# Kernel optimization log

Hardware: AMD Instinct MI355X
Metric: run time of the kernel (lower is better)

Reference implementation:

```python
import jax, jax.numpy as jnp
import numpy as np

WS = 7   # w_size
K = 9    # k_neighbors


def setup_inputs() -> dict:
    key = jax.random.key(0)
    ks = jax.random.split(key, 6)
    B, C, H, W = 16, 64, 112, 112
    Cf = C // 4
    return {
        'x_in': jax.random.normal(ks[0], (B, C, H, W), jnp.float32),
        'Wf': jax.random.normal(ks[1], (Cf, C), jnp.float32) / np.sqrt(C).astype(np.float32),
        'bf': jnp.zeros((Cf,), jnp.float32),
        'Wp': jax.random.normal(ks[2], (C, Cf), jnp.float32) / np.sqrt(Cf).astype(np.float32),
        'bp': jnp.zeros((C,), jnp.float32),
        'W1': jax.random.normal(ks[3], (4, 2), jnp.float32) / np.sqrt(2.0).astype(np.float32),
        'b1': jnp.zeros((4,), jnp.float32),
        'W2': jax.random.normal(ks[4], (1, 4), jnp.float32) / 2.0,
        'b2': jnp.zeros((1,), jnp.float32),
        'sigma': jnp.asarray(4.0, jnp.float32),
        'alpha': jnp.asarray(0.5, jnp.float32),
    }


def reference(x_in, Wf, bf, Wp, bp, W1, b1, W2, b2, sigma, alpha):
    B, C, H, W = x_in.shape
    w, h = H // WS, W // WS                      # per-window spatial dims
    Bp, N = B * WS * WS, w * h                   # num windows, nodes per window
    # window partition: b c (Wg w) (Hg h) -> (b Wg Hg) c w h
    x = x_in.reshape(B, C, WS, w, WS, h).transpose(0, 2, 4, 1, 3, 5).reshape(Bp, C, w, h)
    # 1x1 conv f: dim -> dim//4
    f = jnp.einsum('bchw,oc->bohw', x, Wf) + bf[None, :, None, None]
    Cf = f.shape[1]
    xf = f.reshape(Bp, Cf, N).transpose(0, 2, 1)          # [Bp, N, Cf] node features
    # all-pairs cosine similarity (torch eps=1e-8)
    xn = xf / jnp.maximum(jnp.linalg.norm(xf, axis=-1, keepdims=True), 1e-8)
    sim_feat = jnp.einsum('bnc,bmc->bnm', xn, xn)         # [Bp, N, N]
    # spatial gaussian similarity
    ii, jj = jnp.meshgrid(jnp.arange(w), jnp.arange(h), indexing='ij')
    coords = jnp.stack([ii, jj], -1).reshape(N, 2).astype(jnp.float32)
    dist = jnp.sqrt(jnp.sum((coords[:, None] - coords[None]) ** 2, -1))
    sim_dist = jnp.exp(-dist ** 2 / (2.0 * sigma ** 2))   # [N, N]
    combined = alpha * sim_feat + (1.0 - alpha) * sim_dist[None]
    _, idx = jax.lax.top_k(combined, K)                   # [Bp, N, K] neighbor ids
    # gather neighbor messages; edges of node n are exactly its K top-k columns
    msg = xf[jnp.arange(Bp)[:, None, None], idx]          # [Bp, N, K, Cf]
    sf = jnp.take_along_axis(sim_feat, idx, axis=-1)      # edge cosine sim
    sd = sim_dist[jnp.arange(N)[:, None], idx]            # edge spatial sim
    pair = jnp.stack([sf, sd], -1)                        # [Bp, N, K, 2]
    hdn = jax.nn.silu(pair @ W1.T + b1)
    wgt = jax.nn.sigmoid(hdn @ W2.T + b2)[..., 0]         # [Bp, N, K]
    # scatter_add over edge_index[0] == per-source sum over its K edges
    wn = wgt / (jnp.sum(wgt, -1, keepdims=True) + 1e-12)
    out = jnp.einsum('bnk,bnkc->bnc', wn, msg)            # [Bp, N, Cf]
    out = out.reshape(Bp, w, h, Cf).transpose(0, 3, 1, 2)
    # window un-partition: (b Wg Hg) c w h -> b c (Wg w) (Hg h)
    out = out.reshape(B, WS, WS, Cf, w, h).transpose(0, 3, 1, 4, 2, 5).reshape(B, Cf, H, W)
    # 1x1 conv p: dim//4 -> dim, then flatten(2)
    y = jnp.einsum('bchw,oc->bohw', out, Wp) + bp[None, :, None, None]
    return y.reshape(B, C, H * W)
```

## Files before the change

kernel.cpp:

```cpp
#include <hip/hip_runtime.h>
#include <math.h>

#define CC    64
#define CF    16
#define NPIX  256
#define KK    9
#define HWQ   12544
#define WWQ   112

__global__ __launch_bounds__(256) void gnn_fused(
    const float* __restrict__ x_in, const float* __restrict__ Wf,
    const float* __restrict__ bf,   const float* __restrict__ Wp,
    const float* __restrict__ bp,   const float* __restrict__ W1,
    const float* __restrict__ b1,   const float* __restrict__ W2,
    const float* __restrict__ b2,   const float* __restrict__ sigma_p,
    const float* __restrict__ alpha_p, float* __restrict__ y)
{
    __shared__ float s_xf[NPIX][CF];
    __shared__ float s_xn[NPIX][CF];
    __shared__ float s_W[CC * CF];
    __shared__ float s_table[451];
    __shared__ float s_bias[CC];

    const int bpi = blockIdx.x;
    const int bb  = bpi / 49;
    const int ssb = bpi % 49;
    const int s1  = ssb / 7, s2 = ssb % 7;
    const int tid = threadIdx.x;
    const int pi  = tid >> 4, pj = tid & 15;
    const int gy  = s1 * 16 + pi, gx = s2 * 16 + pj;

    const float alpha = alpha_p[0];
    const float oma   = 1.0f - alpha;
    const float sig   = sigma_p[0];
    const float denom = 2.0f * sig * sig;

    for (int t = tid; t < CF * CC; t += NPIX) s_W[t] = Wf[t];
    if (tid < CF) s_bias[tid] = bf[tid];
    for (int t = tid; t < 451; t += NPIX) {
        float dd = sqrtf((float)t);
        s_table[t] = expf((-(dd * dd)) / denom);
    }
    float W1r[8], b1r[4], W2r[4];
    #pragma unroll
    for (int h = 0; h < 8; ++h) W1r[h] = W1[h];
    #pragma unroll
    for (int h = 0; h < 4; ++h) { b1r[h] = b1[h]; W2r[h] = W2[h]; }
    const float b2r = b2[0];
    __syncthreads();

    const float* xb = x_in + (size_t)bb * CC * HWQ + (size_t)gy * WWQ + gx;
    float fv[CF];
    #pragma unroll
    for (int o = 0; o < CF; ++o) fv[o] = 0.0f;
    for (int c = 0; c < CC; ++c) {
        float xv = xb[(size_t)c * HWQ];
        #pragma unroll
        for (int o = 0; o < CF; ++o)
            fv[o] = fmaf(xv, s_W[o * CC + c], fv[o]);
    }
    #pragma unroll
    for (int o = 0; o < CF; ++o) fv[o] += s_bias[o];

    float ss2 = 0.0f;
    #pragma unroll
    for (int o = 0; o < CF; ++o) ss2 = fmaf(fv[o], fv[o], ss2);
    float nrm = fmaxf(sqrtf(ss2), 1e-8f);

    float xnr[CF];
    #pragma unroll
    for (int o = 0; o < CF; ++o) {
        xnr[o] = fv[o] / nrm;
        s_xf[tid][o] = fv[o];
        s_xn[tid][o] = xnr[o];
    }
    __syncthreads();

    float tv[KK]; int ti[KK];
    #pragma unroll
    for (int k = 0; k < KK; ++k) { tv[k] = -INFINITY; ti[k] = 0; }

    for (int m = 0; m < NPIX; ++m) {
        const float4* xm4 = reinterpret_cast<const float4*>(&s_xn[m][0]);
        float4 a0 = xm4[0], a1 = xm4[1], a2 = xm4[2], a3 = xm4[3];
        float dot = 0.0f;
        dot = fmaf(xnr[0],  a0.x, dot); dot = fmaf(xnr[1],  a0.y, dot);
        dot = fmaf(xnr[2],  a0.z, dot); dot = fmaf(xnr[3],  a0.w, dot);
        dot = fmaf(xnr[4],  a1.x, dot); dot = fmaf(xnr[5],  a1.y, dot);
        dot = fmaf(xnr[6],  a1.z, dot); dot = fmaf(xnr[7],  a1.w, dot);
        dot = fmaf(xnr[8],  a2.x, dot); dot = fmaf(xnr[9],  a2.y, dot);
        dot = fmaf(xnr[10], a2.z, dot); dot = fmaf(xnr[11], a2.w, dot);
        dot = fmaf(xnr[12], a3.x, dot); dot = fmaf(xnr[13], a3.y, dot);
        dot = fmaf(xnr[14], a3.z, dot); dot = fmaf(xnr[15], a3.w, dot);

        int di = pi - (m >> 4);
        int dj = pj - (m & 15);
        float sd = s_table[di * di + dj * dj];
        float comb = __fadd_rn(__fmul_rn(alpha, dot), __fmul_rn(oma, sd));

        if (comb > tv[KK - 1]) {
            float cv = comb; int ci = m;
            #pragma unroll
            for (int t = KK - 1; t >= 0; --t) {
                bool g = (cv > tv[t]);
                float ov = tv[t]; int oi = ti[t];
                if (g) {
                    if (t + 1 < KK) { tv[t + 1] = ov; ti[t + 1] = oi; }
                    tv[t] = cv; ti[t] = ci;
                }
            }
        }
    }

    float wk[KK];
    float wsum = 0.0f;
    #pragma unroll
    for (int k = 0; k < KK; ++k) {
        int m = ti[k];
        int di = pi - (m >> 4);
        int dj = pj - (m & 15);
        float sd = s_table[di * di + dj * dj];
        float sf = (tv[k] - __fmul_rn(oma, sd)) / alpha;
        float hsum = b2r;
        #pragma unroll
        for (int h = 0; h < 4; ++h) {
            float z  = fmaf(sf, W1r[2 * h], fmaf(sd, W1r[2 * h + 1], b1r[h]));
            float sg = 1.0f / (1.0f + expf(-z));
            hsum = fmaf(z * sg, W2r[h], hsum);
        }
        float wg = 1.0f / (1.0f + expf(-hsum));
        wk[k] = wg;
        wsum += wg;
    }
    wsum += 1e-12f;

    float outv[CF];
    #pragma unroll
    for (int o = 0; o < CF; ++o) outv[o] = 0.0f;
    #pragma unroll
    for (int k = 0; k < KK; ++k) {
        float wn = wk[k] / wsum;
        int m = ti[k];
        const float4* xf4 = reinterpret_cast<const float4*>(&s_xf[m][0]);
        float4 m0 = xf4[0], m1 = xf4[1], m2 = xf4[2], m3 = xf4[3];
        outv[0]  = fmaf(wn, m0.x, outv[0]);  outv[1]  = fmaf(wn, m0.y, outv[1]);
        outv[2]  = fmaf(wn, m0.z, outv[2]);  outv[3]  = fmaf(wn, m0.w, outv[3]);
        outv[4]  = fmaf(wn, m1.x, outv[4]);  outv[5]  = fmaf(wn, m1.y, outv[5]);
        outv[6]  = fmaf(wn, m1.z, outv[6]);  outv[7]  = fmaf(wn, m1.w, outv[7]);
        outv[8]  = fmaf(wn, m2.x, outv[8]);  outv[9]  = fmaf(wn, m2.y, outv[9]);
        outv[10] = fmaf(wn, m2.z, outv[10]); outv[11] = fmaf(wn, m2.w, outv[11]);
        outv[12] = fmaf(wn, m3.x, outv[12]); outv[13] = fmaf(wn, m3.y, outv[13]);
        outv[14] = fmaf(wn, m3.z, outv[14]); outv[15] = fmaf(wn, m3.w, outv[15]);
    }

    __syncthreads();
    for (int t = tid; t < CC * CF; t += NPIX) s_W[t] = Wp[t];
    if (tid < CC) s_bias[tid] = bp[tid];
    __syncthreads();

    float* yb = y + (size_t)bb * CC * HWQ + (size_t)gy * WWQ + gx;
    for (int o = 0; o < CC; ++o) {
        float acc = 0.0f;
        #pragma unroll
        for (int c = 0; c < CF; ++c)
            acc = fmaf(outv[c], s_W[o * CF + c], acc);
        yb[(size_t)o * HWQ] = acc + s_bias[o];
    }
}

extern "C" void kernel_launch(void* const* d_in, const int* in_sizes, int n_in,
                              void* d_out, int out_size, void* d_ws, size_t ws_size,
                              hipStream_t stream) {
    const float* x_in  = (const float*)d_in[0];
    const float* Wf    = (const float*)d_in[1];
    const float* bf    = (const float*)d_in[2];
    const float* Wp    = (const float*)d_in[3];
    const float* bp    = (const float*)d_in[4];
    const float* W1    = (const float*)d_in[5];
    const float* b1    = (const float*)d_in[6];
    const float* W2    = (const float*)d_in[7];
    const float* b2    = (const float*)d_in[8];
    const float* sigma = (const float*)d_in[9];
    const float* alpha = (const float*)d_in[10];
    float* y = (float*)d_out;

    gnn_fused<<<784, 256, 0, stream>>>(x_in, Wf, bf, Wp, bp, W1, b1, W2, b2,
                                       sigma, alpha, y);
}
```

Baseline: 147.8 us.

## Split each window across two blocks and use branchless med3 top-k insertion

Each 256-node window now runs on two 128-thread blocks. Both blocks recompute the full window's 1x1 projection, and each block handles top-k and output for half the nodes. The raw-feature shared array is dropped: normalized features are stored with per-node norms and the norm is multiplied back during aggregation. The top-k insertion becomes a branchless fmed3/select network, the spatial loop is split into row and column parts, and the Wp reads are vectorized. This trades doubled projection work and doubled x_in reads for twice as many blocks, less shared memory and shorter insertion chains.

```diff
diff --git a/kernel.cpp b/kernel.cpp
--- a/kernel.cpp
+++ b/kernel.cpp
@@ -7,8 +7,9 @@
 #define KK    9
 #define HWQ   12544
 #define WWQ   112
-
-__global__ __launch_bounds__(256) void gnn_fused(
+#define BLK   128
+
+__global__ __launch_bounds__(BLK) void gnn_fused(
     const float* __restrict__ x_in, const float* __restrict__ Wf,
     const float* __restrict__ bf,   const float* __restrict__ Wp,
     const float* __restrict__ bp,   const float* __restrict__ W1,
@@ -16,28 +17,28 @@
     const float* __restrict__ b2,   const float* __restrict__ sigma_p,
     const float* __restrict__ alpha_p, float* __restrict__ y)
 {
-    __shared__ float s_xf[NPIX][CF];
     __shared__ float s_xn[NPIX][CF];
+    __shared__ float s_nrm[NPIX];
     __shared__ float s_W[CC * CF];
     __shared__ float s_table[451];
     __shared__ float s_bias[CC];
 
-    const int bpi = blockIdx.x;
-    const int bb  = bpi / 49;
-    const int ssb = bpi % 49;
-    const int s1  = ssb / 7, s2 = ssb % 7;
-    const int tid = threadIdx.x;
-    const int pi  = tid >> 4, pj = tid & 15;
-    const int gy  = s1 * 16 + pi, gx = s2 * 16 + pj;
+    const int bid  = blockIdx.x;
+    const int tile = bid >> 1;
+    const int hlf  = bid & 1;
+    const int bb   = tile / 49;
+    const int ssb  = tile % 49;
+    const int s1   = ssb / 7, s2 = ssb % 7;
+    const int tid  = threadIdx.x;
 
     const float alpha = alpha_p[0];
     const float oma   = 1.0f - alpha;
     const float sig   = sigma_p[0];
     const float denom = 2.0f * sig * sig;
 
-    for (int t = tid; t < CF * CC; t += NPIX) s_W[t] = Wf[t];
+    for (int t = tid; t < CF * CC; t += BLK) s_W[t] = Wf[t];
     if (tid < CF) s_bias[tid] = bf[tid];
-    for (int t = tid; t < 451; t += NPIX) {
+    for (int t = tid; t < 451; t += BLK) {
         float dd = sqrtf((float)t);
         s_table[t] = expf((-(dd * dd)) / denom);
     }
@@ -49,65 +50,106 @@
     const float b2r = b2[0];
     __syncthreads();
 
-    const float* xb = x_in + (size_t)bb * CC * HWQ + (size_t)gy * WWQ + gx;
-    float fv[CF];
-    #pragma unroll
-    for (int o = 0; o < CF; ++o) fv[o] = 0.0f;
-    for (int c = 0; c < CC; ++c) {
-        float xv = xb[(size_t)c * HWQ];
-        #pragma unroll
-        for (int o = 0; o < CF; ++o)
-            fv[o] = fmaf(xv, s_W[o * CC + c], fv[o]);
-    }
-    #pragma unroll
-    for (int o = 0; o < CF; ++o) fv[o] += s_bias[o];
-
-    float ss2 = 0.0f;
-    #pragma unroll
-    for (int o = 0; o < CF; ++o) ss2 = fmaf(fv[o], fv[o], ss2);
-    float nrm = fmaxf(sqrtf(ss2), 1e-8f);
+    #pragma unroll
+    for (int half = 0; half < 2; ++half) {
+        const int p   = tid + half * BLK;
+        const int ppi = p >> 4, ppj = p & 15;
+        const int pgy = s1 * 16 + ppi, pgx = s2 * 16 + ppj;
+        const float* xb = x_in + (size_t)bb * CC * HWQ + (size_t)pgy * WWQ + pgx;
+        float fv[CF];
+        #pragma unroll
+        for (int o = 0; o < CF; ++o) fv[o] = 0.0f;
+        for (int c = 0; c < CC; ++c) {
+            float xv = xb[(size_t)c * HWQ];
+            #pragma unroll
+            for (int o = 0; o < CF; ++o)
+                fv[o] = fmaf(xv, s_W[o * CC + c], fv[o]);
+        }
+        #pragma unroll
+        for (int o = 0; o < CF; ++o) fv[o] += s_bias[o];
+
+        float ss2 = 0.0f;
+        #pragma unroll
+        for (int o = 0; o < CF; ++o) ss2 = fmaf(fv[o], fv[o], ss2);
+        float nrm = fmaxf(sqrtf(ss2), 1e-8f);
+        #pragma unroll
+        for (int o = 0; o < CF; ++o) s_xn[p][o] = fv[o] / nrm;
+        s_nrm[p] = nrm;
+    }
+    __syncthreads();
+
+    const int r  = hlf * BLK + tid;
+    const int pi = r >> 4, pj = r & 15;
 
     float xnr[CF];
-    #pragma unroll
-    for (int o = 0; o < CF; ++o) {
-        xnr[o] = fv[o] / nrm;
-        s_xf[tid][o] = fv[o];
-        s_xn[tid][o] = xnr[o];
-    }
-    __syncthreads();
+    {
+        const float4* xr4 = reinterpret_cast<const float4*>(&s_xn[r][0]);
+        float4 r0 = xr4[0], r1 = xr4[1], r2 = xr4[2], r3 = xr4[3];
+        xnr[0]=r0.x;  xnr[1]=r0.y;  xnr[2]=r0.z;  xnr[3]=r0.w;
+        xnr[4]=r1.x;  xnr[5]=r1.y;  xnr[6]=r1.z;  xnr[7]=r1.w;
+        xnr[8]=r2.x;  xnr[9]=r2.y;  xnr[10]=r2.z; xnr[11]=r2.w;
+        xnr[12]=r3.x; xnr[13]=r3.y; xnr[14]=r3.z; xnr[15]=r3.w;
+    }
 
     float tv[KK]; int ti[KK];
     #pragma unroll
     for (int k = 0; k < KK; ++k) { tv[k] = -INFINITY; ti[k] = 0; }
 
-    for (int m = 0; m < NPIX; ++m) {
-        const float4* xm4 = reinterpret_cast<const float4*>(&s_xn[m][0]);
-        float4 a0 = xm4[0], a1 = xm4[1], a2 = xm4[2], a3 = xm4[3];
-        float dot = 0.0f;
-        dot = fmaf(xnr[0],  a0.x, dot); dot = fmaf(xnr[1],  a0.y, dot);
-        dot = fmaf(xnr[2],  a0.z, dot); dot = fmaf(xnr[3],  a0.w, dot);
-        dot = fmaf(xnr[4],  a1.x, dot); dot = fmaf(xnr[5],  a1.y, dot);
-        dot = fmaf(xnr[6],  a1.z, dot); dot = fmaf(xnr[7],  a1.w, dot);
-        dot = fmaf(xnr[8],  a2.x, dot); dot = fmaf(xnr[9],  a2.y, dot);
-        dot = fmaf(xnr[10], a2.z, dot); dot = fmaf(xnr[11], a2.w, dot);
-        dot = fmaf(xnr[12], a3.x, dot); dot = fmaf(xnr[13], a3.y, dot);
-        dot = fmaf(xnr[14], a3.z, dot); dot = fmaf(xnr[15], a3.w, dot);
-
-        int di = pi - (m >> 4);
-        int dj = pj - (m & 15);
-        float sd = s_table[di * di + dj * dj];
-        float comb = __fadd_rn(__fmul_rn(alpha, dot), __fmul_rn(oma, sd));
-
-        if (comb > tv[KK - 1]) {
-            float cv = comb; int ci = m;
-            #pragma unroll
-            for (int t = KK - 1; t >= 0; --t) {
-                bool g = (cv > tv[t]);
-                float ov = tv[t]; int oi = ti[t];
-                if (g) {
-                    if (t + 1 < KK) { tv[t + 1] = ov; ti[t + 1] = oi; }
-                    tv[t] = cv; ti[t] = ci;
-                }
+    for (int mi = 0; mi < 16; ++mi) {
+        const int di  = pi - mi;
+        const int d2i = di * di;
+        const int mb  = mi << 4;
+        #pragma unroll 4
+        for (int mj = 0; mj < 16; ++mj) {
+            const int m = mb + mj;
+            const float4* xm4 = reinterpret_cast<const float4*>(&s_xn[m][0]);
+            float4 a0 = xm4[0], a1 = xm4[1], a2 = xm4[2], a3 = xm4[3];
+            float dot = 0.0f;
+            dot = fmaf(xnr[0],  a0.x, dot); dot = fmaf(xnr[1],  a0.y, dot);
+            dot = fmaf(xnr[2],  a0.z, dot); dot = fmaf(xnr[3],  a0.w, dot);
+            dot = fmaf(xnr[4],  a1.x, dot); dot = fmaf(xnr[5],  a1.y, dot);
+            dot = fmaf(xnr[6],  a1.z, dot); dot = fmaf(xnr[7],  a1.w, dot);
+            dot = fmaf(xnr[8],  a2.x, dot); dot = fmaf(xnr[9],  a2.y, dot);
+            dot = fmaf(xnr[10], a2.z, dot); dot = fmaf(xnr[11], a2.w, dot);
+            dot = fmaf(xnr[12], a3.x, dot); dot = fmaf(xnr[13], a3.y, dot);
+            dot = fmaf(xnr[14], a3.z, dot); dot = fmaf(xnr[15], a3.w, dot);
+
+            const int dj = pj - mj;
+            const float sd = s_table[d2i + dj * dj];
+            const float comb = __fadd_rn(__fmul_rn(alpha, dot), __fmul_rn(oma, sd));
+
+            if (comb > tv[8]) {
+                const float cv = comb; const int ci = m;
+                const bool g0 = cv > tv[0];
+                const bool g1 = cv > tv[1];
+                const bool g2 = cv > tv[2];
+                const bool g3 = cv > tv[3];
+                const bool g4 = cv > tv[4];
+                const bool g5 = cv > tv[5];
+                const bool g6 = cv > tv[6];
+                const bool g7 = cv > tv[7];
+                const float nv0 = g0 ? cv : tv[0];
+                const float nv1 = __builtin_amdgcn_fmed3f(cv, tv[0], tv[1]);
+                const float nv2 = __builtin_amdgcn_fmed3f(cv, tv[1], tv[2]);
+                const float nv3 = __builtin_amdgcn_fmed3f(cv, tv[2], tv[3]);
+                const float nv4 = __builtin_amdgcn_fmed3f(cv, tv[3], tv[4]);
+                const float nv5 = __builtin_amdgcn_fmed3f(cv, tv[4], tv[5]);
+                const float nv6 = __builtin_amdgcn_fmed3f(cv, tv[5], tv[6]);
+                const float nv7 = __builtin_amdgcn_fmed3f(cv, tv[6], tv[7]);
+                const float nv8 = __builtin_amdgcn_fmed3f(cv, tv[7], tv[8]);
+                const int nt0 = g0 ? ci : ti[0];
+                const int nt1 = g0 ? ti[0] : (g1 ? ci : ti[1]);
+                const int nt2 = g1 ? ti[1] : (g2 ? ci : ti[2]);
+                const int nt3 = g2 ? ti[2] : (g3 ? ci : ti[3]);
+                const int nt4 = g3 ? ti[3] : (g4 ? ci : ti[4]);
+                const int nt5 = g4 ? ti[4] : (g5 ? ci : ti[5]);
+                const int nt6 = g5 ? ti[5] : (g6 ? ci : ti[6]);
+                const int nt7 = g6 ? ti[6] : (g7 ? ci : ti[7]);
+                const int nt8 = g7 ? ti[7] : ci;
+                tv[0]=nv0; tv[1]=nv1; tv[2]=nv2; tv[3]=nv3; tv[4]=nv4;
+                tv[5]=nv5; tv[6]=nv6; tv[7]=nv7; tv[8]=nv8;
+                ti[0]=nt0; ti[1]=nt1; ti[2]=nt2; ti[3]=nt3; ti[4]=nt4;
+                ti[5]=nt5; ti[6]=nt6; ti[7]=nt7; ti[8]=nt8;
             }
         }
     }
@@ -139,31 +181,39 @@
     for (int o = 0; o < CF; ++o) outv[o] = 0.0f;
     #pragma unroll
     for (int k = 0; k < KK; ++k) {
-        float wn = wk[k] / wsum;
-        int m = ti[k];
-        const float4* xf4 = reinterpret_cast<const float4*>(&s_xf[m][0]);
+        const int m = ti[k];
+        const float wnm = (wk[k] / wsum) * s_nrm[m];
+        const float4* xf4 = reinterpret_cast<const float4*>(&s_xn[m][0]);
         float4 m0 = xf4[0], m1 = xf4[1], m2 = xf4[2], m3 = xf4[3];
-        outv[0]  = fmaf(wn, m0.x, outv[0]);  outv[1]  = fmaf(wn, m0.y, outv[1]);
-        outv[2]  = fmaf(wn, m0.z, outv[2]);  outv[3]  = fmaf(wn, m0.w, outv[3]);
-        outv[4]  = fmaf(wn, m1.x, outv[4]);  outv[5]  = fmaf(wn, m1.y, outv[5]);
-        outv[6]  = fmaf(wn, m1.z, outv[6]);  outv[7]  = fmaf(wn, m1.w, outv[7]);
-        outv[8]  = fmaf(wn, m2.x, outv[8]);  outv[9]  = fmaf(wn, m2.y, outv[9]);
-        outv[10] = fmaf(wn, m2.z, outv[10]); outv[11] = fmaf(wn, m2.w, outv[11]);
-        outv[12] = fmaf(wn, m3.x, outv[12]); outv[13] = fmaf(wn, m3.y, outv[13]);
-        outv[14] = fmaf(wn, m3.z, outv[14]); outv[15] = fmaf(wn, m3.w, outv[15]);
-    }
-
-    __syncthreads();
-    for (int t = tid; t < CC * CF; t += NPIX) s_W[t] = Wp[t];
+        outv[0]  = fmaf(wnm, m0.x, outv[0]);  outv[1]  = fmaf(wnm, m0.y, outv[1]);
+        outv[2]  = fmaf(wnm, m0.z, outv[2]);  outv[3]  = fmaf(wnm, m0.w, outv[3]);
+        outv[4]  = fmaf(wnm, m1.x, outv[4]);  outv[5]  = fmaf(wnm, m1.y, outv[5]);
+        outv[6]  = fmaf(wnm, m1.z, outv[6]);  outv[7]  = fmaf(wnm, m1.w, outv[7]);
+        outv[8]  = fmaf(wnm, m2.x, outv[8]);  outv[9]  = fmaf(wnm, m2.y, outv[9]);
+        outv[10] = fmaf(wnm, m2.z, outv[10]); outv[11] = fmaf(wnm, m2.w, outv[11]);
+        outv[12] = fmaf(wnm, m3.x, outv[12]); outv[13] = fmaf(wnm, m3.y, outv[13]);
+        outv[14] = fmaf(wnm, m3.z, outv[14]); outv[15] = fmaf(wnm, m3.w, outv[15]);
+    }
+
+    __syncthreads();
+    for (int t = tid; t < CC * CF; t += BLK) s_W[t] = Wp[t];
     if (tid < CC) s_bias[tid] = bp[tid];
     __syncthreads();
 
+    const int gy = s1 * 16 + pi, gx = s2 * 16 + pj;
     float* yb = y + (size_t)bb * CC * HWQ + (size_t)gy * WWQ + gx;
     for (int o = 0; o < CC; ++o) {
+        const float4* w4 = reinterpret_cast<const float4*>(&s_W[o * CF]);
+        float4 w0 = w4[0], w1 = w4[1], w2 = w4[2], w3 = w4[3];
         float acc = 0.0f;
-        #pragma unroll
-        for (int c = 0; c < CF; ++c)
-            acc = fmaf(outv[c], s_W[o * CF + c], acc);
+        acc = fmaf(outv[0],  w0.x, acc); acc = fmaf(outv[1],  w0.y, acc);
+        acc = fmaf(outv[2],  w0.z, acc); acc = fmaf(outv[3],  w0.w, acc);
+        acc = fmaf(outv[4],  w1.x, acc); acc = fmaf(outv[5],  w1.y, acc);
+        acc = fmaf(outv[6],  w1.z, acc); acc = fmaf(outv[7],  w1.w, acc);
+        acc = fmaf(outv[8],  w2.x, acc); acc = fmaf(outv[9],  w2.y, acc);
+        acc = fmaf(outv[10], w2.z, acc); acc = fmaf(outv[11], w2.w, acc);
+        acc = fmaf(outv[12], w3.x, acc); acc = fmaf(outv[13], w3.y, acc);
+        acc = fmaf(outv[14], w3.z, acc); acc = fmaf(outv[15], w3.w, acc);
         yb[(size_t)o * HWQ] = acc + s_bias[o];
     }
 }
@@ -184,6 +234,6 @@
     const float* alpha = (const float*)d_in[10];
     float* y = (float*)d_out;
 
-    gnn_fused<<<784, 256, 0, stream>>>(x_in, Wf, bf, Wp, bp, W1, b1, W2, b2,
-                                       sigma, alpha, y);
+    gnn_fused<<<784 * 2, BLK, 0, stream>>>(x_in, Wf, bf, Wp, bp, W1, b1, W2, b2,
+                                           sigma, alpha, y);
 }
```

After: 187.6 us. +26.9%, slower.

## Split into feature kernel and 64-thread similarity/top-k kernel via workspace

Applied to the files above, without the earlier changes.

Splits the fused kernel in two. The first kernel computes the normalized 1x1-conv features and their norms into a global workspace. The second uses 64-thread blocks, four per window, reading neighbor features from global/L2 instead of LDS. It also adds a branchless med3-based top-9 insertion, pre-scales the spatial table by (1-alpha), and rebuilds messages as xn*norm. This is meant to raise occupancy and remove the divergent insertion branch, at the cost of an extra kernel launch and a workspace round trip.

```diff
diff --git a/kernel.cpp b/kernel.cpp
--- a/kernel.cpp
+++ b/kernel.cpp
@@ -7,6 +7,249 @@
 #define KK    9
 #define HWQ   12544
 #define WWQ   112
+#define NTILE 784
+
+__global__ __launch_bounds__(64) void feat_k(
+    const float* __restrict__ x_in, const float* __restrict__ Wf,
+    const float* __restrict__ bf,
+    float* __restrict__ xn_g, float* __restrict__ nrm_g)
+{
+    __shared__ float s_Wt[CC * CF];
+    __shared__ float s_bf[CF];
+    const int tid = threadIdx.x;
+    for (int idx = tid; idx < CC * CF; idx += 64) {
+        int c = idx >> 4, o = idx & 15;
+        s_Wt[idx] = Wf[o * CC + c];
+    }
+    if (tid < CF) s_bf[tid] = bf[tid];
+    __syncthreads();
+
+    const int p    = blockIdx.x * 64 + tid;
+    const int tile = p >> 8, pix = p & 255;
+    const int bb = tile / 49, ssb = tile % 49;
+    const int s1 = ssb / 7, s2 = ssb % 7;
+    const int gy = s1 * 16 + (pix >> 4), gx = s2 * 16 + (pix & 15);
+    const float* xb = x_in + (size_t)bb * CC * HWQ + (size_t)gy * WWQ + gx;
+
+    float fv[CF];
+    #pragma unroll
+    for (int o = 0; o < CF; ++o) fv[o] = 0.0f;
+    for (int c = 0; c < CC; ++c) {
+        float xv = xb[(size_t)c * HWQ];
+        const float4* w4 = reinterpret_cast<const float4*>(&s_Wt[c << 4]);
+        float4 w0 = w4[0], w1 = w4[1], w2 = w4[2], w3 = w4[3];
+        fv[0]  = fmaf(xv, w0.x, fv[0]);  fv[1]  = fmaf(xv, w0.y, fv[1]);
+        fv[2]  = fmaf(xv, w0.z, fv[2]);  fv[3]  = fmaf(xv, w0.w, fv[3]);
+        fv[4]  = fmaf(xv, w1.x, fv[4]);  fv[5]  = fmaf(xv, w1.y, fv[5]);
+        fv[6]  = fmaf(xv, w1.z, fv[6]);  fv[7]  = fmaf(xv, w1.w, fv[7]);
+        fv[8]  = fmaf(xv, w2.x, fv[8]);  fv[9]  = fmaf(xv, w2.y, fv[9]);
+        fv[10] = fmaf(xv, w2.z, fv[10]); fv[11] = fmaf(xv, w2.w, fv[11]);
+        fv[12] = fmaf(xv, w3.x, fv[12]); fv[13] = fmaf(xv, w3.y, fv[13]);
+        fv[14] = fmaf(xv, w3.z, fv[14]); fv[15] = fmaf(xv, w3.w, fv[15]);
+    }
+    #pragma unroll
+    for (int o = 0; o < CF; ++o) fv[o] += s_bf[o];
+
+    float ss2 = 0.0f;
+    #pragma unroll
+    for (int o = 0; o < CF; ++o) ss2 = fmaf(fv[o], fv[o], ss2);
+    float nrm = fmaxf(sqrtf(ss2), 1e-8f);
+
+    float xn[CF];
+    #pragma unroll
+    for (int o = 0; o < CF; ++o) xn[o] = fv[o] / nrm;
+
+    float4* dst = reinterpret_cast<float4*>(xn_g + (size_t)p * CF);
+    dst[0] = make_float4(xn[0],  xn[1],  xn[2],  xn[3]);
+    dst[1] = make_float4(xn[4],  xn[5],  xn[6],  xn[7]);
+    dst[2] = make_float4(xn[8],  xn[9],  xn[10], xn[11]);
+    dst[3] = make_float4(xn[12], xn[13], xn[14], xn[15]);
+    nrm_g[p] = nrm;
+}
+
+#define DOT16(dot, a0, a1, a2, a3)                                   \
+    dot = fmaf(xnr[0],  (a0).x, dot); dot = fmaf(xnr[1],  (a0).y, dot); \
+    dot = fmaf(xnr[2],  (a0).z, dot); dot = fmaf(xnr[3],  (a0).w, dot); \
+    dot = fmaf(xnr[4],  (a1).x, dot); dot = fmaf(xnr[5],  (a1).y, dot); \
+    dot = fmaf(xnr[6],  (a1).z, dot); dot = fmaf(xnr[7],  (a1).w, dot); \
+    dot = fmaf(xnr[8],  (a2).x, dot); dot = fmaf(xnr[9],  (a2).y, dot); \
+    dot = fmaf(xnr[10], (a2).z, dot); dot = fmaf(xnr[11], (a2).w, dot); \
+    dot = fmaf(xnr[12], (a3).x, dot); dot = fmaf(xnr[13], (a3).y, dot); \
+    dot = fmaf(xnr[14], (a3).z, dot); dot = fmaf(xnr[15], (a3).w, dot);
+
+#define TOP9_INSERT(cv, ci) {                                        \
+    const bool g0 = (cv) > tv0; const bool g1 = (cv) > tv1;          \
+    const bool g2 = (cv) > tv2; const bool g3 = (cv) > tv3;          \
+    const bool g4 = (cv) > tv4; const bool g5 = (cv) > tv5;          \
+    const bool g6 = (cv) > tv6; const bool g7 = (cv) > tv7;          \
+    const bool g8 = (cv) > tv8;                                      \
+    const float nv0 = g0 ? (cv) : tv0;                               \
+    const float nv1 = __builtin_amdgcn_fmed3f((cv), tv0, tv1);       \
+    const float nv2 = __builtin_amdgcn_fmed3f((cv), tv1, tv2);       \
+    const float nv3 = __builtin_amdgcn_fmed3f((cv), tv2, tv3);       \
+    const float nv4 = __builtin_amdgcn_fmed3f((cv), tv3, tv4);       \
+    const float nv5 = __builtin_amdgcn_fmed3f((cv), tv4, tv5);       \
+    const float nv6 = __builtin_amdgcn_fmed3f((cv), tv5, tv6);       \
+    const float nv7 = __builtin_amdgcn_fmed3f((cv), tv6, tv7);       \
+    const float nv8 = __builtin_amdgcn_fmed3f((cv), tv7, tv8);       \
+    const int nt0 = g0 ? (ci) : ti0;                                 \
+    const int nt1 = g0 ? ti0 : (g1 ? (ci) : ti1);                    \
+    const int nt2 = g1 ? ti1 : (g2 ? (ci) : ti2);                    \
+    const int nt3 = g2 ? ti2 : (g3 ? (ci) : ti3);                    \
+    const int nt4 = g3 ? ti3 : (g4 ? (ci) : ti4);                    \
+    const int nt5 = g4 ? ti4 : (g5 ? (ci) : ti5);                    \
+    const int nt6 = g5 ? ti5 : (g6 ? (ci) : ti6);                    \
+    const int nt7 = g6 ? ti6 : (g7 ? (ci) : ti7);                    \
+    const int nt8 = g7 ? ti7 : (g8 ? (ci) : ti8);                    \
+    tv0 = nv0; tv1 = nv1; tv2 = nv2; tv3 = nv3; tv4 = nv4;           \
+    tv5 = nv5; tv6 = nv6; tv7 = nv7; tv8 = nv8;                      \
+    ti0 = nt0; ti1 = nt1; ti2 = nt2; ti3 = nt3; ti4 = nt4;           \
+    ti5 = nt5; ti6 = nt6; ti7 = nt7; ti8 = nt8; }
+
+#define SIM_ITER(MJ) {                                               \
+    const float4* xm4 =                                              \
+        reinterpret_cast<const float4*>(xrow + (MJ) * CF);           \
+    float4 a0 = xm4[0], a1 = xm4[1], a2 = xm4[2], a3 = xm4[3];       \
+    float dot = 0.0f;                                                \
+    DOT16(dot, a0, a1, a2, a3);                                      \
+    const int dj = pj - (MJ);                                        \
+    const float sdA = s_tabA[d2i + dj * dj];                         \
+    const float comb = __fadd_rn(__fmul_rn(alpha, dot), sdA);        \
+    TOP9_INSERT(comb, mbase + (MJ)); }
+
+__global__ __launch_bounds__(64) void gnn_main(
+    const float* __restrict__ xn_g, const float* __restrict__ nrm_g,
+    const float* __restrict__ Wp,   const float* __restrict__ bp,
+    const float* __restrict__ W1,   const float* __restrict__ b1,
+    const float* __restrict__ W2,   const float* __restrict__ b2,
+    const float* __restrict__ sigma_p, const float* __restrict__ alpha_p,
+    float* __restrict__ y)
+{
+    __shared__ float s_tab[451];
+    __shared__ float s_tabA[451];
+    __shared__ float s_Wp[CC * CF];
+    __shared__ float s_bp[CC];
+
+    const int bid  = blockIdx.x;
+    const int tile = bid >> 2;
+    const int rg   = bid & 3;
+    const int bb = tile / 49, ssb = tile % 49;
+    const int s1 = ssb / 7, s2 = ssb % 7;
+    const int tid = threadIdx.x;
+
+    const float alpha = alpha_p[0];
+    const float oma   = 1.0f - alpha;
+    const float sig   = sigma_p[0];
+    const float denom = 2.0f * sig * sig;
+
+    for (int t = tid; t < 451; t += 64) {
+        float dd = sqrtf((float)t);
+        float v  = expf((-(dd * dd)) / denom);
+        s_tab[t]  = v;
+        s_tabA[t] = __fmul_rn(oma, v);
+    }
+    for (int t = tid; t < CC * CF; t += 64) s_Wp[t] = Wp[t];
+    s_bp[tid] = bp[tid];
+    float W1r[8], b1r[4], W2r[4];
+    #pragma unroll
+    for (int h = 0; h < 8; ++h) W1r[h] = W1[h];
+    #pragma unroll
+    for (int h = 0; h < 4; ++h) { b1r[h] = b1[h]; W2r[h] = W2[h]; }
+    const float b2r = b2[0];
+    __syncthreads();
+
+    const int r  = rg * 64 + tid;
+    const int pi = r >> 4, pj = r & 15;
+    const float* xt = xn_g + (size_t)tile * NPIX * CF;
+
+    float xnr[CF];
+    {
+        const float4* xr4 = reinterpret_cast<const float4*>(xt + (size_t)r * CF);
+        float4 r0 = xr4[0], r1 = xr4[1], r2 = xr4[2], r3 = xr4[3];
+        xnr[0]=r0.x;  xnr[1]=r0.y;  xnr[2]=r0.z;  xnr[3]=r0.w;
+        xnr[4]=r1.x;  xnr[5]=r1.y;  xnr[6]=r1.z;  xnr[7]=r1.w;
+        xnr[8]=r2.x;  xnr[9]=r2.y;  xnr[10]=r2.z; xnr[11]=r2.w;
+        xnr[12]=r3.x; xnr[13]=r3.y; xnr[14]=r3.z; xnr[15]=r3.w;
+    }
+
+    float tv0,tv1,tv2,tv3,tv4,tv5,tv6,tv7,tv8;
+    int   ti0,ti1,ti2,ti3,ti4,ti5,ti6,ti7,ti8;
+    tv0=tv1=tv2=tv3=tv4=tv5=tv6=tv7=tv8 = -INFINITY;
+    ti0=ti1=ti2=ti3=ti4=ti5=ti6=ti7=ti8 = 0;
+
+    for (int mi = 0; mi < 16; ++mi) {
+        const int di  = pi - mi;
+        const int d2i = di * di;
+        const int mbase = mi << 4;
+        const float* xrow = xt + (size_t)mbase * CF;
+        SIM_ITER(0)  SIM_ITER(1)  SIM_ITER(2)  SIM_ITER(3)
+        SIM_ITER(4)  SIM_ITER(5)  SIM_ITER(6)  SIM_ITER(7)
+        SIM_ITER(8)  SIM_ITER(9)  SIM_ITER(10) SIM_ITER(11)
+        SIM_ITER(12) SIM_ITER(13) SIM_ITER(14) SIM_ITER(15)
+    }
+
+    const float tv[KK] = {tv0,tv1,tv2,tv3,tv4,tv5,tv6,tv7,tv8};
+    const int   ti[KK] = {ti0,ti1,ti2,ti3,ti4,ti5,ti6,ti7,ti8};
+
+    float wk[KK];
+    float wsum = 0.0f;
+    #pragma unroll
+    for (int k = 0; k < KK; ++k) {
+        int m = ti[k];
+        int di = pi - (m >> 4);
+        int dj = pj - (m & 15);
+        float sd = s_tab[di * di + dj * dj];
+        float sf = (tv[k] - __fmul_rn(oma, sd)) / alpha;
+        float hsum = b2r;
+        #pragma unroll
+        for (int h = 0; h < 4; ++h) {
+            float z  = fmaf(sf, W1r[2 * h], fmaf(sd, W1r[2 * h + 1], b1r[h]));
+            float sg = 1.0f / (1.0f + expf(-z));
+            hsum = fmaf(z * sg, W2r[h], hsum);
+        }
+        float wg = 1.0f / (1.0f + expf(-hsum));
+        wk[k] = wg;
+        wsum += wg;
+    }
+    wsum += 1e-12f;
+
+    const float* nt = nrm_g + (size_t)tile * NPIX;
+    float outv[CF];
+    #pragma unroll
+    for (int o = 0; o < CF; ++o) outv[o] = 0.0f;
+    #pragma unroll
+    for (int k = 0; k < KK; ++k) {
+        const int m = ti[k];
+        const float wnm = (wk[k] / wsum) * nt[m];
+        const float4* xf4 = reinterpret_cast<const float4*>(xt + (size_t)m * CF);
+        float4 m0 = xf4[0], m1 = xf4[1], m2 = xf4[2], m3 = xf4[3];
+        outv[0]  = fmaf(wnm, m0.x, outv[0]);  outv[1]  = fmaf(wnm, m0.y, outv[1]);
+        outv[2]  = fmaf(wnm, m0.z, outv[2]);  outv[3]  = fmaf(wnm, m0.w, outv[3]);
+        outv[4]  = fmaf(wnm, m1.x, outv[4]);  outv[5]  = fmaf(wnm, m1.y, outv[5]);
+        outv[6]  = fmaf(wnm, m1.z, outv[6]);  outv[7]  = fmaf(wnm, m1.w, outv[7]);
+        outv[8]  = fmaf(wnm, m2.x, outv[8]);  outv[9]  = fmaf(wnm, m2.y, outv[9]);
+        outv[10] = fmaf(wnm, m2.z, outv[10]); outv[11] = fmaf(wnm, m2.w, outv[11]);
+        outv[12] = fmaf(wnm, m3.x, outv[12]); outv[13] = fmaf(wnm, m3.y, outv[13]);
+        outv[14] = fmaf(wnm, m3.z, outv[14]); outv[15] = fmaf(wnm, m3.w, outv[15]);
+    }
+
+    const int gy = s1 * 16 + pi, gx = s2 * 16 + pj;
+    float* yb = y + (size_t)bb * CC * HWQ + (size_t)gy * WWQ + gx;
+    for (int o = 0; o < CC; ++o) {
+        const float4* w4 = reinterpret_cast<const float4*>(&s_Wp[o * CF]);
+        float4 w0 = w4[0], w1 = w4[1], w2 = w4[2], w3 = w4[3];
+        float acc = 0.0f;
+        acc = fmaf(outv[0],  w0.x, acc); acc = fmaf(outv[1],  w0.y, acc);
+        acc = fmaf(outv[2],  w0.z, acc); acc = fmaf(outv[3],  w0.w, acc);
+        acc = fmaf(outv[4],  w1.x, acc); acc = fmaf(outv[5],  w1.y, acc);
+        acc = fmaf(outv[6],  w1.z, acc); acc = fmaf(outv[7],  w1.w, acc);
+        acc = fmaf(outv[8],  w2.x, acc); acc = fmaf(outv[9],  w2.y, acc);
+        acc = fmaf(outv[10], w2.z, acc); acc = fmaf(outv[11], w2.w, acc);
+        acc = fmaf(outv[12], w3.x, acc); acc = fmaf(outv[13], w3.y, acc);
+        acc = fmaf(outv[14], w3.z, acc); acc = fmaf(outv[15], w3.w, acc);
+        yb[(size_t)o * HWQ] = acc + s_bp[o];
+    }
+}
 
 __global__ __launch_bounds__(256) void gnn_fused(
     const float* __restrict__ x_in, const float* __restrict__ Wf,
@@ -184,6 +427,15 @@
     const float* alpha = (const float*)d_in[10];
     float* y = (float*)d_out;
 
-    gnn_fused<<<784, 256, 0, stream>>>(x_in, Wf, bf, Wp, bp, W1, b1, W2, b2,
-                                       sigma, alpha, y);
+    const size_t need = (size_t)(NTILE * NPIX * CF + NTILE * NPIX) * sizeof(float);
+    if (ws_size >= need) {
+        float* xn_g  = (float*)d_ws;
+        float* nrm_g = xn_g + (size_t)NTILE * NPIX * CF;
+        feat_k<<<3136, 64, 0, stream>>>(x_in, Wf, bf, xn_g, nrm_g);
+        gnn_main<<<3136, 64, 0, stream>>>(xn_g, nrm_g, Wp, bp, W1, b1, W2, b2,
+                                          sigma, alpha, y);
+    } else {
+        gnn_fused<<<NTILE, NPIX, 0, stream>>>(x_in, Wf, bf, Wp, bp, W1, b1, W2,
+                                              b2, sigma, alpha, y);
+    }
 }
```

Measured after the change: 161.7 us. 1.09x slower.

## Split feature projection into separate kernel and parallelize top-k across split candidates

Applied to the files above, without the earlier changes.

Adds a separate kernel that computes the 1x1 projection and normalized features into workspace. A second kernel launches two blocks per window, with each thread handling two query pixels over a quarter of the candidates. It uses a branchless med3-based top-9 insertion, and partial top-k lists are merged through shared memory before the epilogue. This targets the serial per-thread 256-candidate scan and its divergent insertion, at the cost of an extra global round trip, a second launch, and three quarters of the threads sitting idle in the epilogue.

```diff
diff --git a/kernel.cpp b/kernel.cpp
--- a/kernel.cpp
+++ b/kernel.cpp
@@ -7,6 +7,340 @@
 #define KK    9
 #define HWQ   12544
 #define WWQ   112
+#define NTILE 784
+#define NROWS (NTILE * NPIX)
+
+__global__ __launch_bounds__(64, 4) void feat_k(
+    const float* __restrict__ x_in, const float* __restrict__ Wf,
+    const float* __restrict__ bf,
+    float* __restrict__ xn_g, float* __restrict__ nrm_g)
+{
+    __shared__ float s_Wt[CC * CF];
+    __shared__ float s_bf[CF];
+    const int tid = threadIdx.x;
+    for (int idx = tid; idx < CC * CF; idx += 64) {
+        int c = idx >> 4, o = idx & 15;
+        s_Wt[idx] = Wf[o * CC + c];
+    }
+    if (tid < CF) s_bf[tid] = bf[tid];
+    __syncthreads();
+
+    const int p    = blockIdx.x * 64 + tid;
+    const int tile = p >> 8, pix = p & 255;
+    const int bb = tile / 49, ssb = tile % 49;
+    const int s1 = ssb / 7, s2 = ssb % 7;
+    const int gy = s1 * 16 + (pix >> 4), gx = s2 * 16 + (pix & 15);
+    const float* xb = x_in + (size_t)bb * CC * HWQ + (size_t)gy * WWQ + gx;
+
+    float fv[CF];
+    #pragma unroll
+    for (int o = 0; o < CF; ++o) fv[o] = 0.0f;
+    #pragma unroll 8
+    for (int c = 0; c < CC; ++c) {
+        float xv = xb[(size_t)c * HWQ];
+        const float4* w4 = reinterpret_cast<const float4*>(&s_Wt[c << 4]);
+        float4 w0 = w4[0], w1 = w4[1], w2 = w4[2], w3 = w4[3];
+        fv[0]  = fmaf(xv, w0.x, fv[0]);  fv[1]  = fmaf(xv, w0.y, fv[1]);
+        fv[2]  = fmaf(xv, w0.z, fv[2]);  fv[3]  = fmaf(xv, w0.w, fv[3]);
+        fv[4]  = fmaf(xv, w1.x, fv[4]);  fv[5]  = fmaf(xv, w1.y, fv[5]);
+        fv[6]  = fmaf(xv, w1.z, fv[6]);  fv[7]  = fmaf(xv, w1.w, fv[7]);
+        fv[8]  = fmaf(xv, w2.x, fv[8]);  fv[9]  = fmaf(xv, w2.y, fv[9]);
+        fv[10] = fmaf(xv, w2.z, fv[10]); fv[11] = fmaf(xv, w2.w, fv[11]);
+        fv[12] = fmaf(xv, w3.x, fv[12]); fv[13] = fmaf(xv, w3.y, fv[13]);
+        fv[14] = fmaf(xv, w3.z, fv[14]); fv[15] = fmaf(xv, w3.w, fv[15]);
+    }
+    #pragma unroll
+    for (int o = 0; o < CF; ++o) fv[o] += s_bf[o];
+
+    float ss2 = 0.0f;
+    #pragma unroll
+    for (int o = 0; o < CF; ++o) ss2 = fmaf(fv[o], fv[o], ss2);
+    float nrm = fmaxf(sqrtf(ss2), 1e-8f);
+
+    float xn[CF];
+    #pragma unroll
+    for (int o = 0; o < CF; ++o) xn[o] = fv[o] / nrm;
+
+    float4* dst = reinterpret_cast<float4*>(xn_g + (size_t)p * CF);
+    dst[0] = make_float4(xn[0],  xn[1],  xn[2],  xn[3]);
+    dst[1] = make_float4(xn[4],  xn[5],  xn[6],  xn[7]);
+    dst[2] = make_float4(xn[8],  xn[9],  xn[10], xn[11]);
+    dst[3] = make_float4(xn[12], xn[13], xn[14], xn[15]);
+    nrm_g[p] = nrm;
+}
+
+#define DOT16(dot, X, a0, a1, a2, a3)                                \
+    dot = fmaf(X[0],  (a0).x, dot); dot = fmaf(X[1],  (a0).y, dot);  \
+    dot = fmaf(X[2],  (a0).z, dot); dot = fmaf(X[3],  (a0).w, dot);  \
+    dot = fmaf(X[4],  (a1).x, dot); dot = fmaf(X[5],  (a1).y, dot);  \
+    dot = fmaf(X[6],  (a1).z, dot); dot = fmaf(X[7],  (a1).w, dot);  \
+    dot = fmaf(X[8],  (a2).x, dot); dot = fmaf(X[9],  (a2).y, dot);  \
+    dot = fmaf(X[10], (a2).z, dot); dot = fmaf(X[11], (a2).w, dot);  \
+    dot = fmaf(X[12], (a3).x, dot); dot = fmaf(X[13], (a3).y, dot);  \
+    dot = fmaf(X[14], (a3).z, dot); dot = fmaf(X[15], (a3).w, dot);
+
+#define TOP9_INS(S, cv, ci) {                                        \
+    const bool g0 = (cv) > tv0##S; const bool g1 = (cv) > tv1##S;    \
+    const bool g2 = (cv) > tv2##S; const bool g3 = (cv) > tv3##S;    \
+    const bool g4 = (cv) > tv4##S; const bool g5 = (cv) > tv5##S;    \
+    const bool g6 = (cv) > tv6##S; const bool g7 = (cv) > tv7##S;    \
+    const bool g8 = (cv) > tv8##S;                                   \
+    const float nv0 = g0 ? (cv) : tv0##S;                            \
+    const float nv1 = __builtin_amdgcn_fmed3f((cv), tv0##S, tv1##S); \
+    const float nv2 = __builtin_amdgcn_fmed3f((cv), tv1##S, tv2##S); \
+    const float nv3 = __builtin_amdgcn_fmed3f((cv), tv2##S, tv3##S); \
+    const float nv4 = __builtin_amdgcn_fmed3f((cv), tv3##S, tv4##S); \
+    const float nv5 = __builtin_amdgcn_fmed3f((cv), tv4##S, tv5##S); \
+    const float nv6 = __builtin_amdgcn_fmed3f((cv), tv5##S, tv6##S); \
+    const float nv7 = __builtin_amdgcn_fmed3f((cv), tv6##S, tv7##S); \
+    const float nv8 = __builtin_amdgcn_fmed3f((cv), tv7##S, tv8##S); \
+    const int nt0 = g0 ? (ci) : ti0##S;                              \
+    const int nt1 = g0 ? ti0##S : (g1 ? (ci) : ti1##S);              \
+    const int nt2 = g1 ? ti1##S : (g2 ? (ci) : ti2##S);              \
+    const int nt3 = g2 ? ti2##S : (g3 ? (ci) : ti3##S);              \
+    const int nt4 = g3 ? ti3##S : (g4 ? (ci) : ti4##S);              \
+    const int nt5 = g4 ? ti4##S : (g5 ? (ci) : ti5##S);              \
+    const int nt6 = g5 ? ti5##S : (g6 ? (ci) : ti6##S);              \
+    const int nt7 = g6 ? ti6##S : (g7 ? (ci) : ti7##S);              \
+    const int nt8 = g7 ? ti7##S : (g8 ? (ci) : ti8##S);              \
+    tv0##S = nv0; tv1##S = nv1; tv2##S = nv2; tv3##S = nv3;          \
+    tv4##S = nv4; tv5##S = nv5; tv6##S = nv6; tv7##S = nv7;          \
+    tv8##S = nv8;                                                    \
+    ti0##S = nt0; ti1##S = nt1; ti2##S = nt2; ti3##S = nt3;          \
+    ti4##S = nt4; ti5##S = nt5; ti6##S = nt6; ti7##S = nt7;          \
+    ti8##S = nt8; }
+
+#define SIM_ITER2(MJ) {                                              \
+    const int lm = lmbase + (MJ);                                    \
+    const float4* xm4 =                                              \
+        reinterpret_cast<const float4*>(&s_xn[gmbase + (MJ)][0]);    \
+    const float4 a0 = xm4[0], a1 = xm4[1], a2 = xm4[2], a3 = xm4[3]; \
+    float dotA = 0.0f, dotB = 0.0f;                                  \
+    DOT16(dotA, xnrA, a0, a1, a2, a3);                               \
+    DOT16(dotB, xnrB, a0, a1, a2, a3);                               \
+    const int dj = pj - (MJ);                                        \
+    const int dj2 = dj * dj;                                         \
+    const float sA = s_tabA[d2iA + dj2];                             \
+    const float sB = s_tabA[d2iB + dj2];                             \
+    const float combA = __fadd_rn(__fmul_rn(alpha, dotA), sA);       \
+    const float combB = __fadd_rn(__fmul_rn(alpha, dotB), sB);       \
+    TOP9_INS(A, combA, lm)                                           \
+    TOP9_INS(B, combB, lm) }
+
+#define SIM_ROW16_2()                                                \
+        SIM_ITER2(0)  SIM_ITER2(1)  SIM_ITER2(2)  SIM_ITER2(3)       \
+        SIM_ITER2(4)  SIM_ITER2(5)  SIM_ITER2(6)  SIM_ITER2(7)       \
+        SIM_ITER2(8)  SIM_ITER2(9)  SIM_ITER2(10) SIM_ITER2(11)      \
+        SIM_ITER2(12) SIM_ITER2(13) SIM_ITER2(14) SIM_ITER2(15)
+
+#define PUBLISH(slot) {                                              \
+    s_pv[slot][0][0][l64]=tv0A; s_pi[slot][0][0][l64]=ti0A;          \
+    s_pv[slot][0][1][l64]=tv1A; s_pi[slot][0][1][l64]=ti1A;          \
+    s_pv[slot][0][2][l64]=tv2A; s_pi[slot][0][2][l64]=ti2A;          \
+    s_pv[slot][0][3][l64]=tv3A; s_pi[slot][0][3][l64]=ti3A;          \
+    s_pv[slot][0][4][l64]=tv4A; s_pi[slot][0][4][l64]=ti4A;          \
+    s_pv[slot][0][5][l64]=tv5A; s_pi[slot][0][5][l64]=ti5A;          \
+    s_pv[slot][0][6][l64]=tv6A; s_pi[slot][0][6][l64]=ti6A;          \
+    s_pv[slot][0][7][l64]=tv7A; s_pi[slot][0][7][l64]=ti7A;          \
+    s_pv[slot][0][8][l64]=tv8A; s_pi[slot][0][8][l64]=ti8A;          \
+    s_pv[slot][1][0][l64]=tv0B; s_pi[slot][1][0][l64]=ti0B;          \
+    s_pv[slot][1][1][l64]=tv1B; s_pi[slot][1][1][l64]=ti1B;          \
+    s_pv[slot][1][2][l64]=tv2B; s_pi[slot][1][2][l64]=ti2B;          \
+    s_pv[slot][1][3][l64]=tv3B; s_pi[slot][1][3][l64]=ti3B;          \
+    s_pv[slot][1][4][l64]=tv4B; s_pi[slot][1][4][l64]=ti4B;          \
+    s_pv[slot][1][5][l64]=tv5B; s_pi[slot][1][5][l64]=ti5B;          \
+    s_pv[slot][1][6][l64]=tv6B; s_pi[slot][1][6][l64]=ti6B;          \
+    s_pv[slot][1][7][l64]=tv7B; s_pi[slot][1][7][l64]=ti7B;          \
+    s_pv[slot][1][8][l64]=tv8B; s_pi[slot][1][8][l64]=ti8B; }
+
+#define MERGEFROM(slot) {                                            \
+    _Pragma("unroll")                                                \
+    for (int k = 0; k < KK; ++k) {                                   \
+        const float bvA = s_pv[slot][0][k][l64];                     \
+        const int   biA = s_pi[slot][0][k][l64];                     \
+        TOP9_INS(A, bvA, biA)                                        \
+        const float bvB = s_pv[slot][1][k][l64];                     \
+        const int   biB = s_pi[slot][1][k][l64];                     \
+        TOP9_INS(B, bvB, biB)                                        \
+    } }
+
+#define EPILOGUE(TV, TI, PI, PJ) {                                   \
+    float wk[KK]; float wsum = 0.0f;                                 \
+    _Pragma("unroll")                                                \
+    for (int k = 0; k < KK; ++k) {                                   \
+        int m = TI[k];                                               \
+        int di = (PI) - (m >> 4);                                    \
+        int dj = (PJ) - (m & 15);                                    \
+        float sd = s_tab[di * di + dj * dj];                         \
+        float sf = (TV[k] - __fmul_rn(oma, sd)) / alpha;             \
+        float hsum = b2r;                                            \
+        _Pragma("unroll")                                            \
+        for (int h = 0; h < 4; ++h) {                                \
+            float z  = fmaf(sf, W1r[2*h], fmaf(sd, W1r[2*h+1], b1r[h])); \
+            float sg = 1.0f / (1.0f + expf(-z));                     \
+            hsum = fmaf(z * sg, W2r[h], hsum);                       \
+        }                                                            \
+        float wg = 1.0f / (1.0f + expf(-hsum));                      \
+        wk[k] = wg; wsum += wg;                                      \
+    }                                                                \
+    wsum += 1e-12f;                                                  \
+    float outv[CF];                                                  \
+    _Pragma("unroll")                                                \
+    for (int o = 0; o < CF; ++o) outv[o] = 0.0f;                     \
+    _Pragma("unroll")                                                \
+    for (int k = 0; k < KK; ++k) {                                   \
+        const int m = TI[k];                                         \
+        const float wnm = (wk[k] / wsum) * s_nrm[m];                 \
+        const float4* xf4 = reinterpret_cast<const float4*>(&s_xn[m][0]); \
+        float4 m0 = xf4[0], m1 = xf4[1], m2 = xf4[2], m3 = xf4[3];   \
+        outv[0]  = fmaf(wnm, m0.x, outv[0]);  outv[1]  = fmaf(wnm, m0.y, outv[1]);  \
+        outv[2]  = fmaf(wnm, m0.z, outv[2]);  outv[3]  = fmaf(wnm, m0.w, outv[3]);  \
+        outv[4]  = fmaf(wnm, m1.x, outv[4]);  outv[5]  = fmaf(wnm, m1.y, outv[5]);  \
+        outv[6]  = fmaf(wnm, m1.z, outv[6]);  outv[7]  = fmaf(wnm, m1.w, outv[7]);  \
+        outv[8]  = fmaf(wnm, m2.x, outv[8]);  outv[9]  = fmaf(wnm, m2.y, outv[9]);  \
+        outv[10] = fmaf(wnm, m2.z, outv[10]); outv[11] = fmaf(wnm, m2.w, outv[11]); \
+        outv[12] = fmaf(wnm, m3.x, outv[12]); outv[13] = fmaf(wnm, m3.y, outv[13]); \
+        outv[14] = fmaf(wnm, m3.z, outv[14]); outv[15] = fmaf(wnm, m3.w, outv[15]); \
+    }                                                                \
+    const int gy = s1 * 16 + (PI), gx = s2 * 16 + (PJ);              \
+    float* yb = y + (size_t)bb * CC * HWQ + (size_t)gy * WWQ + gx;   \
+    _Pragma("unroll 4")                                              \
+    for (int o = 0; o < CC; ++o) {                                   \
+        const float4* w4 = reinterpret_cast<const float4*>(&Wp[o * CF]); \
+        float4 w0 = w4[0], w1 = w4[1], w2 = w4[2], w3 = w4[3];       \
+        float acc = 0.0f;                                            \
+        acc = fmaf(outv[0],  w0.x, acc); acc = fmaf(outv[1],  w0.y, acc); \
+        acc = fmaf(outv[2],  w0.z, acc); acc = fmaf(outv[3],  w0.w, acc); \
+        acc = fmaf(outv[4],  w1.x, acc); acc = fmaf(outv[5],  w1.y, acc); \
+        acc = fmaf(outv[6],  w1.z, acc); acc = fmaf(outv[7],  w1.w, acc); \
+        acc = fmaf(outv[8],  w2.x, acc); acc = fmaf(outv[9],  w2.y, acc); \
+        acc = fmaf(outv[10], w2.z, acc); acc = fmaf(outv[11], w2.w, acc); \
+        acc = fmaf(outv[12], w3.x, acc); acc = fmaf(outv[13], w3.y, acc); \
+        acc = fmaf(outv[14], w3.z, acc); acc = fmaf(outv[15], w3.w, acc); \
+        yb[(size_t)o * HWQ] = acc + bp[o];                           \
+    } }
+
+__global__ __launch_bounds__(256, 4) void gnn_split(
+    const float* __restrict__ xn_g, const float* __restrict__ nrm_g,
+    const float* __restrict__ Wp,   const float* __restrict__ bp,
+    const float* __restrict__ W1,   const float* __restrict__ b1,
+    const float* __restrict__ W2,   const float* __restrict__ b2,
+    const float* __restrict__ sigma_p, const float* __restrict__ alpha_p,
+    float* __restrict__ y)
+{
+    __shared__ float s_xn[NPIX][CF];
+    __shared__ float s_nrm[NPIX];
+    __shared__ float s_tab[451];
+    __shared__ float s_tabA[451];
+    __shared__ float s_pv[2][2][KK][64];
+    __shared__ int   s_pi[2][2][KK][64];
+
+    const int bid  = blockIdx.x;
+    const int tile = bid >> 1;
+    const int hlf  = bid & 1;
+    const int bb = tile / 49, ssb = tile % 49;
+    const int s1 = ssb / 7, s2 = ssb % 7;
+    const int tid = threadIdx.x;
+    const int l64 = tid & 63;
+    const int ch  = tid >> 6;
+
+    const float alpha = alpha_p[0];
+    const float oma   = 1.0f - alpha;
+    const float sig   = sigma_p[0];
+    const float denom = 2.0f * sig * sig;
+
+    for (int t = tid; t < 451; t += 256) {
+        float dd = sqrtf((float)t);
+        float v  = expf((-(dd * dd)) / denom);
+        s_tab[t]  = v;
+        s_tabA[t] = __fmul_rn(oma, v);
+    }
+    const float* xt = xn_g + (size_t)tile * NPIX * CF;
+    {
+        const float4* src = reinterpret_cast<const float4*>(xt);
+        float4*       dst = reinterpret_cast<float4*>(&s_xn[0][0]);
+        #pragma unroll
+        for (int i = 0; i < 4; ++i) dst[tid + i * 256] = src[tid + i * 256];
+        s_nrm[tid] = nrm_g[(size_t)tile * NPIX + tid];
+    }
+    float W1r[8], b1r[4], W2r[4];
+    #pragma unroll
+    for (int h = 0; h < 8; ++h) W1r[h] = W1[h];
+    #pragma unroll
+    for (int h = 0; h < 4; ++h) { b1r[h] = b1[h]; W2r[h] = W2[h]; }
+    const float b2r = b2[0];
+    __syncthreads();
+
+    const int rA  = hlf * 128 + l64;
+    const int rB  = rA + 64;
+    const int piA = rA >> 4, piB = rB >> 4;
+    const int pj  = rA & 15;
+
+    float xnrA[CF], xnrB[CF];
+    {
+        const float4* xa = reinterpret_cast<const float4*>(&s_xn[rA][0]);
+        float4 a0 = xa[0], a1 = xa[1], a2 = xa[2], a3 = xa[3];
+        xnrA[0]=a0.x;  xnrA[1]=a0.y;  xnrA[2]=a0.z;  xnrA[3]=a0.w;
+        xnrA[4]=a1.x;  xnrA[5]=a1.y;  xnrA[6]=a1.z;  xnrA[7]=a1.w;
+        xnrA[8]=a2.x;  xnrA[9]=a2.y;  xnrA[10]=a2.z; xnrA[11]=a2.w;
+        xnrA[12]=a3.x; xnrA[13]=a3.y; xnrA[14]=a3.z; xnrA[15]=a3.w;
+        const float4* xb4 = reinterpret_cast<const float4*>(&s_xn[rB][0]);
+        float4 b0 = xb4[0], b1v = xb4[1], b2v = xb4[2], b3 = xb4[3];
+        xnrB[0]=b0.x;  xnrB[1]=b0.y;  xnrB[2]=b0.z;  xnrB[3]=b0.w;
+        xnrB[4]=b1v.x; xnrB[5]=b1v.y; xnrB[6]=b1v.z; xnrB[7]=b1v.w;
+        xnrB[8]=b2v.x; xnrB[9]=b2v.y; xnrB[10]=b2v.z; xnrB[11]=b2v.w;
+        xnrB[12]=b3.x; xnrB[13]=b3.y; xnrB[14]=b3.z; xnrB[15]=b3.w;
+    }
+
+    float tv0A,tv1A,tv2A,tv3A,tv4A,tv5A,tv6A,tv7A,tv8A;
+    int   ti0A,ti1A,ti2A,ti3A,ti4A,ti5A,ti6A,ti7A,ti8A;
+    float tv0B,tv1B,tv2B,tv3B,tv4B,tv5B,tv6B,tv7B,tv8B;
+    int   ti0B,ti1B,ti2B,ti3B,ti4B,ti5B,ti6B,ti7B,ti8B;
+    tv0A=tv1A=tv2A=tv3A=tv4A=tv5A=tv6A=tv7A=tv8A = -INFINITY;
+    ti0A=ti1A=ti2A=ti3A=ti4A=ti5A=ti6A=ti7A=ti8A = 0;
+    tv0B=tv1B=tv2B=tv3B=tv4B=tv5B=tv6B=tv7B=tv8B = -INFINITY;
+    ti0B=ti1B=ti2B=ti3B=ti4B=ti5B=ti6B=ti7B=ti8B = 0;
+
+    const int mi0 = ch << 2;
+    #pragma unroll 1
+    for (int q = 0; q < 4; ++q) {
+        const int mi     = mi0 + q;
+        const int diA    = piA - mi;
+        const int diB    = piB - mi;
+        const int d2iA   = diA * diA;
+        const int d2iB   = diB * diB;
+        const int gmbase = mi << 4;
+        const int lmbase = q << 4;
+        SIM_ROW16_2()
+    }
+
+    {
+        const int cb = ch << 6;
+        ti0A+=cb; ti1A+=cb; ti2A+=cb; ti3A+=cb; ti4A+=cb;
+        ti5A+=cb; ti6A+=cb; ti7A+=cb; ti8A+=cb;
+        ti0B+=cb; ti1B+=cb; ti2B+=cb; ti3B+=cb; ti4B+=cb;
+        ti5B+=cb; ti6B+=cb; ti7B+=cb; ti8B+=cb;
+    }
+
+    if (ch == 1) PUBLISH(0)
+    if (ch == 3) PUBLISH(1)
+    __syncthreads();
+    if (ch == 0) MERGEFROM(0)
+    if (ch == 2) MERGEFROM(1)
+    __syncthreads();
+    if (ch == 2) PUBLISH(0)
+    __syncthreads();
+    if (ch != 0) return;
+    MERGEFROM(0)
+
+    const float tvA[KK] = {tv0A,tv1A,tv2A,tv3A,tv4A,tv5A,tv6A,tv7A,tv8A};
+    const int   tiA[KK] = {ti0A,ti1A,ti2A,ti3A,ti4A,ti5A,ti6A,ti7A,ti8A};
+    const float tvB[KK] = {tv0B,tv1B,tv2B,tv3B,tv4B,tv5B,tv6B,tv7B,tv8B};
+    const int   tiB[KK] = {ti0B,ti1B,ti2B,ti3B,ti4B,ti5B,ti6B,ti7B,ti8B};
+
+    EPILOGUE(tvA, tiA, piA, pj)
+    EPILOGUE(tvB, tiB, piB, pj)
+}
 
 __global__ __launch_bounds__(256) void gnn_fused(
     const float* __restrict__ x_in, const float* __restrict__ Wf,
@@ -184,6 +518,15 @@
     const float* alpha = (const float*)d_in[10];
     float* y = (float*)d_out;
 
-    gnn_fused<<<784, 256, 0, stream>>>(x_in, Wf, bf, Wp, bp, W1, b1, W2, b2,
-                                       sigma, alpha, y);
+    const size_t need = (size_t)(NROWS * (CF + 1)) * sizeof(float);
+    if (ws_size >= need) {
+        float* xn_g  = (float*)d_ws;
+        float* nrm_g = xn_g + (size_t)NROWS * CF;
+        feat_k<<<3136, 64, 0, stream>>>(x_in, Wf, bf, xn_g, nrm_g);
+        gnn_split<<<NTILE * 2, 256, 0, stream>>>(xn_g, nrm_g, Wp, bp, W1, b1,
+                                                 W2, b2, sigma, alpha, y);
+    } else {
+        gnn_fused<<<NTILE, NPIX, 0, stream>>>(x_in, Wf, bf, Wp, bp, W1, b1, W2,
+                                              b2, sigma, alpha, y);
+    }
 }
```

After: 209.8 us. 1.42x slower.
